# Performance work log

Hardware: AMD Instinct MI355X
Metric: run time of the kernel (lower is better)

Reference implementation:

```python
import jax, jax.numpy as jnp
import numpy as np

N_NODES = 50000
N_EDGES = 800000
IN_DIM = 162
HID = 256  # layer_1_feats == layer_2_feats (required by the stack op)


def _lin(k, fan_in, fan_out):
    kw, kb = jax.random.split(k)
    bound = 1.0 / np.sqrt(fan_in)
    w = jax.random.uniform(kw, (fan_in, fan_out), jnp.float32, -bound, bound)
    b = jax.random.uniform(kb, (fan_out,), jnp.float32, -bound, bound)
    return w, b


def setup_inputs() -> dict:
    key = jax.random.key(0)
    ks = jax.random.split(key, 12)
    feat = jax.random.normal(ks[0], (N_NODES, IN_DIM), jnp.float32)
    edge_index = jax.random.randint(ks[1], (2, N_EDGES), 0, N_NODES, jnp.int64)
    g0_w, g0_b = _lin(ks[2], IN_DIM, HID)
    g1_w, g1_b = _lin(ks[3], HID, HID)
    g2_w, g2_b = _lin(ks[4], HID, HID)
    gl_w, gl_b = _lin(ks[5], HID, HID)
    m1a_w, m1a_b = _lin(ks[6], IN_DIM, HID)
    m1b_w, m1b_b = _lin(ks[7], HID, HID)
    m2a_w, m2a_b = _lin(ks[8], HID, HID)
    m2b_w, m2b_b = _lin(ks[9], HID, HID)
    return dict(feat=feat, edge_index=edge_index,
                g0_w=g0_w, g0_b=g0_b, g1_w=g1_w, g1_b=g1_b,
                g2_w=g2_w, g2_b=g2_b, gl_w=gl_w, gl_b=gl_b,
                m1a_w=m1a_w, m1a_b=m1a_b, m1b_w=m1b_w, m1b_b=m1b_b,
                m2a_w=m2a_w, m2a_b=m2a_b, m2b_w=m2b_w, m2b_b=m2b_b)


def _gin_conv(x, src, dst, wa, ba, wb, bb):
    # DGL GINConv('sum'), eps=0: h = MLP(x + sum_{u->v} x[u])
    agg = jax.ops.segment_sum(x[src], dst, num_segments=N_NODES)
    h = jax.nn.relu((x + agg) @ wa + ba)
    return jax.nn.relu(h @ wb + bb)


def reference(feat, edge_index, g0_w, g0_b, g1_w, g1_b, g2_w, g2_b,
              gl_w, gl_b, m1a_w, m1a_b, m1b_w, m1b_b, m2a_w, m2a_b,
              m2b_w, m2b_b):
    src, dst = edge_index[0], edge_index[1]
    # layer-0 graph embedding from raw features
    g_emb0 = jax.nn.relu(jnp.sum(feat, 0) @ g0_w + g0_b)
    # GIN layer 1
    node1 = _gin_conv(feat, src, dst, m1a_w, m1a_b, m1b_w, m1b_b)
    g_emb1 = jax.nn.relu(jnp.sum(node1, 0) @ g1_w + g1_b)
    # GIN layer 2
    node2 = _gin_conv(node1, src, dst, m2a_w, m2a_b, m2b_w, m2b_b)
    g_emb2 = jax.nn.relu(jnp.sum(node2, 0) @ g2_w + g2_b)
    # sum of per-layer graph embeddings -> last linear
    g_sum = g_emb0 + g_emb1 + g_emb2
    g_last = jax.nn.relu(g_sum @ gl_w + gl_b)
    return node2 + g_last  # broadcast [N, HID] + [HID]
```

## Files before the change

### kernel.cpp

```cpp
#include <hip/hip_runtime.h>

#define N_NODES 50000
#define N_EDGES 800000
#define IN_DIM  162
#define HID     256
#define KPAD1   192
#define NB      ((N_NODES + 255) / 256)

typedef __bf16 bf16;
typedef __bf16 bf16x8 __attribute__((ext_vector_type(8)));
typedef __bf16 bf16x4 __attribute__((ext_vector_type(4)));
typedef float  f32x4  __attribute__((ext_vector_type(4)));
typedef float  f32x8  __attribute__((ext_vector_type(8)));
typedef float  f32x16 __attribute__((ext_vector_type(16)));

__device__ __forceinline__ void wf_one(const float* W, bf16* Wf, int K, int E)
{
    int e    = E & 7;
    int lane = (E >> 3) & 63;
    int fb   = (E >> 9) & 15;
    int ks   = E >> 13;
    int n = (fb >> 1) * 32 + (lane & 31);
    int k = ks * 32 + (fb & 1) * 16 + (lane >> 5) * 8 + e;
    Wf[E] = (k < K) ? (bf16)W[(size_t)k * HID + n] : (bf16)0.0f;
}

#define WTB  ((HID * KPAD1 + 3 * HID * HID + 255) / 256)
#define FPB  ((N_NODES + 63) / 64)
#define DGB  (N_EDGES / 256)

__global__ void prep_all(const float* __restrict__ m1aw, const float* __restrict__ m1bw,
                         const float* __restrict__ m2aw, const float* __restrict__ m2bw,
                         bf16* __restrict__ Wf1, bf16* __restrict__ Wf2,
                         bf16* __restrict__ Wf3, bf16* __restrict__ Wf4,
                         const float* __restrict__ feat, bf16* __restrict__ featbf,
                         float* __restrict__ colsum8,
                         const int* __restrict__ dst, int* __restrict__ deg)
{
    __shared__ bf16  tile[64][208];
    __shared__ float pcs[4][KPAD1];

    const int b   = blockIdx.x;
    const int tid = threadIdx.x;

    if (b < WTB) {
        const int R1 = HID * KPAD1;
        const int R2 = HID * HID;
        int idx = b * 256 + tid;
        if (idx < R1)                 wf_one(m1aw, Wf1, IN_DIM, idx);
        else if (idx < R1 + R2)       wf_one(m1bw, Wf2, HID, idx - R1);
        else if (idx < R1 + 2 * R2)   wf_one(m2aw, Wf3, HID, idx - R1 - R2);
        else if (idx < R1 + 3 * R2)   wf_one(m2bw, Wf4, HID, idx - R1 - 2 * R2);
        return;
    }
    if (b < WTB + FPB) {
        const int fp = b - WTB;
        const int r0 = fp * 64;

        if (tid < 192) {
            const int ch = tid % 48;
            const int rg = tid / 48;
            const int c4 = ch * 4;
            float a0 = 0.0f, a1 = 0.0f, a2 = 0.0f, a3 = 0.0f;
#pragma unroll 4
            for (int k = 0; k < 16; ++k) {
                const int rl = rg * 16 + k;
                const int r  = r0 + rl;
                bf16x4 o;
                if (r < N_NODES) {
                    const float* fr = feat + (size_t)r * IN_DIM;
                    float f0 = (c4 + 0 < IN_DIM) ? fr[c4 + 0] : 0.0f;
                    float f1 = (c4 + 1 < IN_DIM) ? fr[c4 + 1] : 0.0f;
                    float f2 = (c4 + 2 < IN_DIM) ? fr[c4 + 2] : 0.0f;
                    float f3 = (c4 + 3 < IN_DIM) ? fr[c4 + 3] : 0.0f;
                    a0 += f0; a1 += f1; a2 += f2; a3 += f3;
                    o[0] = (bf16)f0; o[1] = (bf16)f1; o[2] = (bf16)f2; o[3] = (bf16)f3;
                } else {
#pragma unroll
                    for (int j = 0; j < 4; ++j) o[j] = (bf16)0.0f;
                }
                *(bf16x4*)(&tile[rl][c4]) = o;
            }
            pcs[rg][c4 + 0] = a0;
            pcs[rg][c4 + 1] = a1;
            pcs[rg][c4 + 2] = a2;
            pcs[rg][c4 + 3] = a3;
        }
        __syncthreads();

#pragma unroll
        for (int i = 0; i < 6; ++i) {
            int m  = i * 256 + tid;
            int g  = m / 192;
            int wg = m - g * 192;
            int eo = wg * 8;
            int rl = eo / 24;
            int cc = eo - rl * 24;
            int r  = r0 + rl;
            if (r < N_NODES) {
                bf16x8 o = *(const bf16x8*)(&tile[rl][g * 24 + cc]);
                *(bf16x8*)(featbf + ((size_t)g * N_NODES + r0) * 24 + (size_t)rl * 24 + cc) = o;
            }
        }

        if (tid < IN_DIM) {
            float s = pcs[0][tid] + pcs[1][tid] + pcs[2][tid] + pcs[3][tid];
            atomicAdd(&colsum8[(fp & 7) * KPAD1 + tid], s);
        }
        return;
    }
    {
        int e = (b - WTB - FPB) * 256 + tid;
        atomicAdd(&deg[dst[e]], 1);
    }
}

__global__ void block_degsum(const int* __restrict__ deg, int* __restrict__ bsum)
{
    __shared__ int s[256];
    int t = threadIdx.x;
    int idx = blockIdx.x * 256 + t;
    int v = (idx < N_NODES) ? deg[idx] : 0;
    s[t] = v;
    __syncthreads();
    for (int off = 128; off > 0; off >>= 1) {
        if (t < off) s[t] += s[t + off];
        __syncthreads();
    }
    if (t == 0) bsum[blockIdx.x] = s[0];
}

__global__ void scan_bsum(const int* __restrict__ bsum, int* __restrict__ gsum)
{
    __shared__ int s[256];
    int t = threadIdx.x;
    int v = (t < NB) ? bsum[t] : 0;
    s[t] = v;
    __syncthreads();
    for (int off = 1; off < 256; off <<= 1) {
        int u = (t >= off) ? s[t - off] : 0;
        __syncthreads();
        s[t] += u;
        __syncthreads();
    }
    gsum[t] = s[t] - v;
}

__global__ void block_scan_write(const int* __restrict__ deg, const int* __restrict__ gsum,
                                 int* __restrict__ rowptr, int* __restrict__ cursor)
{
    __shared__ int s[256];
    int t = threadIdx.x;
    int idx = blockIdx.x * 256 + t;
    int v = (idx < N_NODES) ? deg[idx] : 0;
    s[t] = v;
    __syncthreads();
    for (int off = 1; off < 256; off <<= 1) {
        int u = (t >= off) ? s[t - off] : 0;
        __syncthreads();
        s[t] += u;
        __syncthreads();
    }
    int excl = s[t] - v + gsum[blockIdx.x];
    if (idx < N_NODES) {
        rowptr[idx] = excl;
        cursor[idx] = excl;
    }
    if (idx == 0) rowptr[N_NODES] = N_EDGES;
}

#define CFT 2048
#define NRANGE ((N_NODES + 7) / 8)

__global__ void csr_fill_b(const int* __restrict__ src, const int* __restrict__ dst,
                           int* __restrict__ cursor, int* __restrict__ csr_src)
{
    const int g    = blockIdx.x & 7;
    const int tile = blockIdx.x >> 3;
    const int lo   = g * NRANGE;
    const int hi   = lo + NRANGE;
    const int e0   = tile * CFT;
#pragma unroll
    for (int i = 0; i < CFT / 256; ++i) {
        int e = e0 + i * 256 + threadIdx.x;
        if (e < N_EDGES) {
            int d = dst[e];
            if (d >= lo && d < hi) {
                int p = atomicAdd(&cursor[d], 1);
                csr_src[p] = src[e];
            }
        }
    }
}

template<int CHUNK, int NACT>
__launch_bounds__(256)
__global__ void gather_v5(const bf16* __restrict__ xin,
                          const int* __restrict__ rowptr,
                          const int* __restrict__ csr_src,
                          bf16* __restrict__ xout)
{
    const int g    = blockIdx.x & 7;
    const int tile = blockIdx.x >> 3;
    const int wv   = threadIdx.x >> 6;
    const int lane = threadIdx.x & 63;
    const int q    = lane >> 4;
    const int j    = lane & 15;
    const int e    = j >> 2;
    const int c4   = j & 3;
    const int n    = tile * 16 + wv * 4 + q;
    const bool valid = (n < N_NODES);
    const bool act   = (c4 < NACT);
    const int  ce    = c4 * 8;
    const bf16* base = xin + (size_t)g * N_NODES * CHUNK;

    int r0 = 0, deg = 0;
    if (valid) {
        r0  = rowptr[n];
        deg = rowptr[n + 1] - r0;
    }

    int a0 = r0 + j;        if (a0 > N_EDGES - 1) a0 = N_EDGES - 1;
    int a1 = r0 + 16 + j;   if (a1 > N_EDGES - 1) a1 = N_EDGES - 1;
    const int i0 = csr_src[a0];
    const int i1 = csr_src[a1];

    f32x8 acc;
#pragma unroll
    for (int t = 0; t < 8; ++t) acc[t] = 0.0f;
    if (valid && e == 0 && act) {
        bf16x8 t0 = *(const bf16x8*)(base + (size_t)n * CHUNK + ce);
#pragma unroll
        for (int t = 0; t < 8; ++t) acc[t] = (float)t0[t];
    }

    const int lb = lane & ~3;

    {
        const int s0 = __shfl(i0, lb + 0, 64);
        const int s1 = __shfl(i0, lb + 1, 64);
        const int s2 = __shfl(i0, lb + 2, 64);
        const int s3 = __shfl(i0, lb + 3, 64);
        const int p0 = 4 * e;
        if (act) {
            bf16x8 u0 = *(const bf16x8*)(base + (size_t)s0 * CHUNK + ce);
            bf16x8 u1 = *(const bf16x8*)(base + (size_t)s1 * CHUNK + ce);
            bf16x8 u2 = *(const bf16x8*)(base + (size_t)s2 * CHUNK + ce);
            bf16x8 u3 = *(const bf16x8*)(base + (size_t)s3 * CHUNK + ce);
            if (p0 + 0 < deg) {
#pragma unroll
                for (int t = 0; t < 8; ++t) acc[t] += (float)u0[t];
            }
            if (p0 + 1 < deg) {
#pragma unroll
                for (int t = 0; t < 8; ++t) acc[t] += (float)u1[t];
            }
            if (p0 + 2 < deg) {
#pragma unroll
                for (int t = 0; t < 8; ++t) acc[t] += (float)u2[t];
            }
            if (p0 + 3 < deg) {
#pragma unroll
                for (int t = 0; t < 8; ++t) acc[t] += (float)u3[t];
            }
        }
    }

    {
        const int s0 = __shfl(i1, lb + 0, 64);
        const int s1 = __shfl(i1, lb + 1, 64);
        const int s2 = __shfl(i1, lb + 2, 64);
        const int s3 = __shfl(i1, lb + 3, 64);
        const int p0 = 16 + 4 * e;
        if (act && p0 < deg) {
            bf16x8 u0 = *(const bf16x8*)(base + (size_t)s0 * CHUNK + ce);
            bf16x8 u1 = *(const bf16x8*)(base + (size_t)s1 * CHUNK + ce);
            bf16x8 u2 = *(const bf16x8*)(base + (size_t)s2 * CHUNK + ce);
            bf16x8 u3 = *(const bf16x8*)(base + (size_t)s3 * CHUNK + ce);
            {
#pragma unroll
                for (int t = 0; t < 8; ++t) acc[t] += (float)u0[t];
            }
            if (p0 + 1 < deg) {
#pragma unroll
                for (int t = 0; t < 8; ++t) acc[t] += (float)u1[t];
            }
            if (p0 + 2 < deg) {
#pragma unroll
                for (int t = 0; t < 8; ++t) acc[t] += (float)u2[t];
            }
            if (p0 + 3 < deg) {
#pragma unroll
                for (int t = 0; t < 8; ++t) acc[t] += (float)u3[t];
            }
        }
    }

    for (int p = 32 + e; p < deg; p += 4) {
        const int s = csr_src[r0 + p];
        if (act) {
            bf16x8 u = *(const bf16x8*)(base + (size_t)s * CHUNK + ce);
#pragma unroll
            for (int t = 0; t < 8; ++t) acc[t] += (float)u[t];
        }
    }

#pragma unroll
    for (int t = 0; t < 8; ++t) {
        acc[t] += __shfl_xor(acc[t], 4, 64);
        acc[t] += __shfl_xor(acc[t], 8, 64);
    }

    if (valid && e == 0 && act) {
        bf16x8 o;
#pragma unroll
        for (int t = 0; t < 8; ++t) o[t] = (bf16)acc[t];
        __builtin_nontemporal_store(o,
            (bf16x8*)(xout + ((size_t)g * N_NODES + n) * CHUNK + ce));
    }
}

template<int KPAD, int ACHUNK, int OCHUNK>
__launch_bounds__(512)
__global__ void gemm_mlp32(const bf16* __restrict__ X,
                           const bf16* __restrict__ Wf1,
                           const float* __restrict__ bias1,
                           const bf16* __restrict__ Wf2,
                           const float* __restrict__ bias2,
                           bf16* __restrict__ out_bf,
                           float* __restrict__ colsum8,
                           int M)
{
    __shared__ __align__(128) bf16 sH[32 * HID];

    const int tid  = threadIdx.x;
    const int w    = tid >> 6;
    const int lane = tid & 63;
    const int p    = lane >> 5;
    const int cn   = lane & 31;
    const int m_base = blockIdx.x * 32;

    int arow = m_base + cn;
    if (arow >= M) arow = M - 1;

    f32x16 acc;
#pragma unroll
    for (int r = 0; r < 16; ++r) acc[r] = 0.0f;

    constexpr int T1 = KPAD / 16;
#pragma unroll
    for (int t = 0; t < T1; ++t) {
        bf16x8 a;
        {
            const int e = t * 16 + p * 8;
            if constexpr (ACHUNK == 0) {
                a = *(const bf16x8*)(X + (size_t)arow * KPAD + e);
            } else {
                const int gch = e / ACHUNK;
                const int off = e - gch * ACHUNK;
                a = *(const bf16x8*)(X + ((size_t)gch * N_NODES + arow) * ACHUNK + off);
            }
        }
        bf16x8 b = *(const bf16x8*)(Wf1 + ((((t >> 1) * 16 + w * 2 + (t & 1)) * 64) + lane) * 8);
        acc = __builtin_amdgcn_mfma_f32_32x32x16_bf16(a, b, acc, 0, 0, 0);
    }

    char* sHb = (char*)sH;
    {
        const int col = w * 32 + cn;
        const float bv = bias1[col];
#pragma unroll
        for (int r = 0; r < 16; ++r) {
            const int rowl = (r & 3) + 8 * (r >> 2) + 4 * p;
            float v = acc[r] + bv;
            v = v > 0.0f ? v : 0.0f;
            int ba = rowl * (HID * 2) + col * 2;
            ba ^= (rowl & 31) << 4;
            *(bf16*)(sHb + ba) = (bf16)v;
        }
    }
    __syncthreads();

#pragma unroll
    for (int r = 0; r < 16; ++r) acc[r] = 0.0f;

    const int hrow = cn;
    const int hswz = (hrow & 31) << 4;
    constexpr int T2 = HID / 16;
#pragma unroll
    for (int t = 0; t < T2; ++t) {
        const int kb = (t * 16 + p * 8) * 2;
        bf16x8 a = *(const bf16x8*)(sHb + ((hrow * (HID * 2) + kb) ^ hswz));
        bf16x8 b = *(const bf16x8*)(Wf2 + ((((t >> 1) * 16 + w * 2 + (t & 1)) * 64) + lane) * 8);
        acc = __builtin_amdgcn_mfma_f32_32x32x16_bf16(a, b, acc, 0, 0, 0);
    }

    {
        const int col = w * 32 + cn;
        const float bv = bias2[col];
        float part = 0.0f;
#pragma unroll
        for (int r = 0; r < 16; ++r) {
            int rl = (r & 3) + 8 * (r >> 2) + 4 * p;
            int mo = m_base + rl;
            if (mo < M) {
                float v = acc[r] + bv;
                v = v > 0.0f ? v : 0.0f;
                if constexpr (OCHUNK == 0)
                    out_bf[(size_t)mo * HID + col] = (bf16)v;
                else
                    out_bf[((size_t)w * N_NODES + mo) * OCHUNK + cn] = (bf16)v;
                part += v;
            }
        }
        if (colsum8) {
            part += __shfl_xor(part, 32, 64);
            if (p == 0) atomicAdd(&colsum8[(blockIdx.x & 7) * HID + col], part);
        }
    }
}

__global__ void graph_head(const float* __restrict__ cs0_8,
                           const float* __restrict__ cs1_8,
                           const float* __restrict__ cs2_8,
                           const float* __restrict__ g0w, const float* __restrict__ g0b,
                           const float* __restrict__ g1w, const float* __restrict__ g1b,
                           const float* __restrict__ g2w, const float* __restrict__ g2b,
                           const float* __restrict__ glw, const float* __restrict__ glb,
                           float* __restrict__ gvec)
{
    __shared__ float v0[IN_DIM], v1[HID], v2[HID], gs[HID];
    int t = threadIdx.x;
    if (t < IN_DIM) {
        float s = 0.0f;
#pragma unroll
        for (int i = 0; i < 8; ++i) s += cs0_8[i * KPAD1 + t];
        v0[t] = s;
    }
    {
        float s1 = 0.0f, s2 = 0.0f;
#pragma unroll
        for (int i = 0; i < 8; ++i) {
            s1 += cs1_8[i * HID + t];
            s2 += cs2_8[i * HID + t];
        }
        v1[t] = s1;
        v2[t] = s2;
    }
    __syncthreads();

    float a0 = 0.0f, a1 = 0.0f, a2 = 0.0f;
    for (int k = 0; k < IN_DIM; ++k) a0 += v0[k] * g0w[k * HID + t];
    for (int k = 0; k < HID; ++k) {
        a1 += v1[k] * g1w[k * HID + t];
        a2 += v2[k] * g2w[k * HID + t];
    }
    float e0 = fmaxf(a0 + g0b[t], 0.0f);
    float e1 = fmaxf(a1 + g1b[t], 0.0f);
    float e2 = fmaxf(a2 + g2b[t], 0.0f);
    gs[t] = e0 + e1 + e2;
    __syncthreads();

    float a3 = 0.0f;
    for (int k = 0; k < HID; ++k) a3 += gs[k] * glw[k * HID + t];
    gvec[t] = fmaxf(a3 + glb[t], 0.0f);
}

__global__ void final_add(const bf16* __restrict__ node2,
                          const float* __restrict__ gvec,
                          float* __restrict__ out)
{
    int idx = blockIdx.x * blockDim.x + threadIdx.x;
    size_t base = (size_t)idx * 4;
    int c = (int)(base & (HID - 1));
    bf16x4 v = *(const bf16x4*)(node2 + base);
    f32x4 g = *(const f32x4*)(gvec + c);
    f32x4 o;
#pragma unroll
    for (int j = 0; j < 4; ++j) o[j] = (float)v[j] + g[j];
    *(f32x4*)(out + base) = o;
}

extern "C" void kernel_launch(void* const* d_in, const int* in_sizes, int n_in,
                              void* d_out, int out_size, void* d_ws, size_t ws_size,
                              hipStream_t stream)
{
    const float* feat = (const float*)d_in[0];
    const int*   ei   = (const int*)d_in[1];
    const int*   src  = ei;
    const int*   dst  = ei + N_EDGES;
    const float* g0w = (const float*)d_in[2],  *g0b = (const float*)d_in[3];
    const float* g1w = (const float*)d_in[4],  *g1b = (const float*)d_in[5];
    const float* g2w = (const float*)d_in[6],  *g2b = (const float*)d_in[7];
    const float* glw = (const float*)d_in[8],  *glb = (const float*)d_in[9];
    const float* m1aw = (const float*)d_in[10], *m1ab = (const float*)d_in[11];
    const float* m1bw = (const float*)d_in[12], *m1bb = (const float*)d_in[13];
    const float* m2aw = (const float*)d_in[14], *m2ab = (const float*)d_in[15];
    const float* m2bw = (const float*)d_in[16], *m2bb = (const float*)d_in[17];
    float* out = (float*)d_out;

    char* ws = (char*)d_ws;
    size_t off = 0;
    auto alloc = [&](size_t bytes) -> void* {
        void* p = ws + off;
        off += (bytes + 255) & ~(size_t)255;
        return p;
    };
    bf16*  featbf = (bf16*)alloc((size_t)N_NODES * KPAD1 * 2);
    bf16*  xsum  = (bf16*) alloc((size_t)N_NODES * KPAD1 * 2);
    bf16*  y2    = (bf16*) alloc((size_t)N_NODES * HID * 2);
    bf16*  node2 = (bf16*) alloc((size_t)N_NODES * HID * 2);
    bf16*  node1 = (bf16*) alloc((size_t)N_NODES * HID * 2);
    bf16*  Wf1   = (bf16*) alloc((size_t)HID * KPAD1 * 2);
    bf16*  Wf2   = (bf16*) alloc((size_t)HID * HID * 2);
    bf16*  Wf3   = (bf16*) alloc((size_t)HID * HID * 2);
    bf16*  Wf4   = (bf16*) alloc((size_t)HID * HID * 2);
    int*   deg     = (int*)alloc((size_t)N_NODES * 4);
    int*   rowptr  = (int*)alloc((size_t)(N_NODES + 1) * 4);
    int*   cursor  = (int*)alloc((size_t)N_NODES * 4);
    int*   csr_src = (int*)alloc((size_t)N_EDGES * 4);
    int*   bsum    = (int*)alloc(256 * 4);
    int*   gsum    = (int*)alloc(256 * 4);
    float* csums   = (float*)alloc((8 * KPAD1 + 8 * HID + 8 * HID + HID) * 4);
    float* colsum0_8 = csums;
    float* colsum1_8 = csums + 8 * KPAD1;
    float* colsum2_8 = csums + 8 * KPAD1 + 8 * HID;
    float* gvec      = csums + 8 * KPAD1 + 16 * HID;

    hipMemsetAsync(csums, 0, (8 * KPAD1 + 16 * HID) * 4, stream);
    hipMemsetAsync(deg, 0, (size_t)N_NODES * 4, stream);

    prep_all<<<WTB + FPB + DGB, 256, 0, stream>>>(
        m1aw, m1bw, m2aw, m2bw, Wf1, Wf2, Wf3, Wf4,
        feat, featbf, colsum0_8, dst, deg);

    block_degsum<<<NB, 256, 0, stream>>>(deg, bsum);
    scan_bsum<<<1, 256, 0, stream>>>(bsum, gsum);
    block_scan_write<<<NB, 256, 0, stream>>>(deg, gsum, rowptr, cursor);
    csr_fill_b<<<((N_EDGES + CFT - 1) / CFT) * 8, 256, 0, stream>>>(src, dst, cursor, csr_src);

    const int gtiles = (N_NODES + 15) / 16;
    gather_v5<24, 3><<<gtiles * 8, 256, 0, stream>>>(featbf, rowptr, csr_src, xsum);

    const int gblocks = (N_NODES + 31) / 32;
    gemm_mlp32<KPAD1, 24, 32><<<gblocks, 512, 0, stream>>>(
        xsum, Wf1, m1ab, Wf2, m1bb, node1, colsum1_8, N_NODES);
    gather_v5<32, 4><<<gtiles * 8, 256, 0, stream>>>(node1, rowptr, csr_src, y2);
    gemm_mlp32<HID, 32, 0><<<gblocks, 512, 0, stream>>>(
        y2, Wf3, m2ab, Wf4, m2bb, node2, colsum2_8, N_NODES);
    graph_head<<<1, 256, 0, stream>>>(colsum0_8, colsum1_8, colsum2_8,
                                      g0w, g0b, g1w, g1b, g2w, g2b, glw, glb, gvec);
    final_add<<<((size_t)N_NODES * HID / 4 + 255) / 256, 256, 0, stream>>>(node2, gvec, out);
    (void)in_sizes; (void)n_in; (void)out_size; (void)ws_size;
}
```

Before: 419.3 us.

## Merge scan kernels, fuse graph head into final add, combine memsets

Replaces the three-kernel degree scan with one 1024-thread kernel where each thread scans 52 entries in registers. Fuses the graph-head MLP into the final broadcast-add: each of 256 blocks recomputes the head redundantly, then grid-strides over the output. Merges the two memsets into one by placing csums right after deg, and skips the second csr_src load when degree is at most 16. The aim is fewer kernel launches and less idle gap between them; the cost is a serial single-block scan and duplicated head work in every block.

```diff
diff --git a/kernel.cpp b/kernel.cpp
--- a/kernel.cpp
+++ b/kernel.cpp
@@ -5,7 +5,6 @@
 #define IN_DIM  162
 #define HID     256
 #define KPAD1   192
-#define NB      ((N_NODES + 255) / 256)
 
 typedef __bf16 bf16;
 typedef __bf16 bf16x8 __attribute__((ext_vector_type(8)));
@@ -115,58 +114,46 @@
     }
 }
 
-__global__ void block_degsum(const int* __restrict__ deg, int* __restrict__ bsum)
-{
-    __shared__ int s[256];
-    int t = threadIdx.x;
-    int idx = blockIdx.x * 256 + t;
-    int v = (idx < N_NODES) ? deg[idx] : 0;
-    s[t] = v;
+#define SCT 52
+__launch_bounds__(1024)
+__global__ void csr_scan(const int* __restrict__ deg,
+                         int* __restrict__ rowptr, int* __restrict__ cursor)
+{
+    __shared__ int s[1024];
+    const int t = threadIdx.x;
+    const int base = t * SCT;
+    int4 v[13];
+    int sum = 0;
+#pragma unroll
+    for (int i = 0; i < 13; ++i) {
+        int idx = base + i * 4;
+        int4 q = *(const int4*)(deg + idx);
+        q.x = (idx + 0 < N_NODES) ? q.x : 0;
+        q.y = (idx + 1 < N_NODES) ? q.y : 0;
+        q.z = (idx + 2 < N_NODES) ? q.z : 0;
+        q.w = (idx + 3 < N_NODES) ? q.w : 0;
+        v[i] = q;
+        sum += q.x + q.y + q.z + q.w;
+    }
+    s[t] = sum;
     __syncthreads();
-    for (int off = 128; off > 0; off >>= 1) {
-        if (t < off) s[t] += s[t + off];
-        __syncthreads();
-    }
-    if (t == 0) bsum[blockIdx.x] = s[0];
-}
-
-__global__ void scan_bsum(const int* __restrict__ bsum, int* __restrict__ gsum)
-{
-    __shared__ int s[256];
-    int t = threadIdx.x;
-    int v = (t < NB) ? bsum[t] : 0;
-    s[t] = v;
-    __syncthreads();
-    for (int off = 1; off < 256; off <<= 1) {
+    for (int off = 1; off < 1024; off <<= 1) {
         int u = (t >= off) ? s[t - off] : 0;
         __syncthreads();
         s[t] += u;
         __syncthreads();
     }
-    gsum[t] = s[t] - v;
-}
-
-__global__ void block_scan_write(const int* __restrict__ deg, const int* __restrict__ gsum,
-                                 int* __restrict__ rowptr, int* __restrict__ cursor)
-{
-    __shared__ int s[256];
-    int t = threadIdx.x;
-    int idx = blockIdx.x * 256 + t;
-    int v = (idx < N_NODES) ? deg[idx] : 0;
-    s[t] = v;
-    __syncthreads();
-    for (int off = 1; off < 256; off <<= 1) {
-        int u = (t >= off) ? s[t - off] : 0;
-        __syncthreads();
-        s[t] += u;
-        __syncthreads();
-    }
-    int excl = s[t] - v + gsum[blockIdx.x];
-    if (idx < N_NODES) {
-        rowptr[idx] = excl;
-        cursor[idx] = excl;
-    }
-    if (idx == 0) rowptr[N_NODES] = N_EDGES;
+    int run = s[t] - sum;
+#pragma unroll
+    for (int i = 0; i < 13; ++i) {
+        int idx = base + i * 4;
+        int4 q = v[i];
+        if (idx + 0 < N_NODES) { rowptr[idx + 0] = run; cursor[idx + 0] = run; run += q.x; }
+        if (idx + 1 < N_NODES) { rowptr[idx + 1] = run; cursor[idx + 1] = run; run += q.y; }
+        if (idx + 2 < N_NODES) { rowptr[idx + 2] = run; cursor[idx + 2] = run; run += q.z; }
+        if (idx + 3 < N_NODES) { rowptr[idx + 3] = run; cursor[idx + 3] = run; run += q.w; }
+    }
+    if (t == 1023) rowptr[N_NODES] = N_EDGES;
 }
 
 #define CFT 2048
@@ -223,7 +210,8 @@
     int a0 = r0 + j;        if (a0 > N_EDGES - 1) a0 = N_EDGES - 1;
     int a1 = r0 + 16 + j;   if (a1 > N_EDGES - 1) a1 = N_EDGES - 1;
     const int i0 = csr_src[a0];
-    const int i1 = csr_src[a1];
+    int i1 = 0;
+    if (deg > 16) i1 = csr_src[a1];
 
     f32x8 acc;
 #pragma unroll
@@ -420,17 +408,19 @@
     }
 }
 
-__global__ void graph_head(const float* __restrict__ cs0_8,
-                           const float* __restrict__ cs1_8,
-                           const float* __restrict__ cs2_8,
-                           const float* __restrict__ g0w, const float* __restrict__ g0b,
-                           const float* __restrict__ g1w, const float* __restrict__ g1b,
-                           const float* __restrict__ g2w, const float* __restrict__ g2b,
-                           const float* __restrict__ glw, const float* __restrict__ glb,
-                           float* __restrict__ gvec)
-{
-    __shared__ float v0[IN_DIM], v1[HID], v2[HID], gs[HID];
-    int t = threadIdx.x;
+__launch_bounds__(256)
+__global__ void final_gh(const float* __restrict__ cs0_8,
+                         const float* __restrict__ cs1_8,
+                         const float* __restrict__ cs2_8,
+                         const float* __restrict__ g0w, const float* __restrict__ g0b,
+                         const float* __restrict__ g1w, const float* __restrict__ g1b,
+                         const float* __restrict__ g2w, const float* __restrict__ g2b,
+                         const float* __restrict__ glw, const float* __restrict__ glb,
+                         const bf16* __restrict__ node2,
+                         float* __restrict__ out)
+{
+    __shared__ float v0[IN_DIM], v1[HID], v2[HID], gs[HID], gv[HID];
+    const int t = threadIdx.x;
     if (t < IN_DIM) {
         float s = 0.0f;
 #pragma unroll
@@ -463,22 +453,19 @@
 
     float a3 = 0.0f;
     for (int k = 0; k < HID; ++k) a3 += gs[k] * glw[k * HID + t];
-    gvec[t] = fmaxf(a3 + glb[t], 0.0f);
-}
-
-__global__ void final_add(const bf16* __restrict__ node2,
-                          const float* __restrict__ gvec,
-                          float* __restrict__ out)
-{
-    int idx = blockIdx.x * blockDim.x + threadIdx.x;
-    size_t base = (size_t)idx * 4;
-    int c = (int)(base & (HID - 1));
-    bf16x4 v = *(const bf16x4*)(node2 + base);
-    f32x4 g = *(const f32x4*)(gvec + c);
-    f32x4 o;
-#pragma unroll
-    for (int j = 0; j < 4; ++j) o[j] = (float)v[j] + g[j];
-    *(f32x4*)(out + base) = o;
+    gv[t] = fmaxf(a3 + glb[t], 0.0f);
+    __syncthreads();
+
+    const int total = N_NODES * HID / 4;
+    for (int q = blockIdx.x * 256 + t; q < total; q += gridDim.x * 256) {
+        size_t bb = (size_t)q * 4;
+        int c = (int)(bb & (HID - 1));
+        bf16x4 v = *(const bf16x4*)(node2 + bb);
+        f32x4 o;
+#pragma unroll
+        for (int jj = 0; jj < 4; ++jj) o[jj] = (float)v[jj] + gv[c + jj];
+        *(f32x4*)(out + bb) = o;
+    }
 }
 
 extern "C" void kernel_launch(void* const* d_in, const int* in_sizes, int n_in,
@@ -515,28 +502,23 @@
     bf16*  Wf2   = (bf16*) alloc((size_t)HID * HID * 2);
     bf16*  Wf3   = (bf16*) alloc((size_t)HID * HID * 2);
     bf16*  Wf4   = (bf16*) alloc((size_t)HID * HID * 2);
-    int*   deg     = (int*)alloc((size_t)N_NODES * 4);
+    int*   deg   = (int*)  alloc((size_t)N_NODES * 4);
+    float* csums = (float*)alloc((8 * KPAD1 + 16 * HID) * 4);
     int*   rowptr  = (int*)alloc((size_t)(N_NODES + 1) * 4);
     int*   cursor  = (int*)alloc((size_t)N_NODES * 4);
     int*   csr_src = (int*)alloc((size_t)N_EDGES * 4);
-    int*   bsum    = (int*)alloc(256 * 4);
-    int*   gsum    = (int*)alloc(256 * 4);
-    float* csums   = (float*)alloc((8 * KPAD1 + 8 * HID + 8 * HID + HID) * 4);
     float* colsum0_8 = csums;
     float* colsum1_8 = csums + 8 * KPAD1;
     float* colsum2_8 = csums + 8 * KPAD1 + 8 * HID;
-    float* gvec      = csums + 8 * KPAD1 + 16 * HID;
-
-    hipMemsetAsync(csums, 0, (8 * KPAD1 + 16 * HID) * 4, stream);
-    hipMemsetAsync(deg, 0, (size_t)N_NODES * 4, stream);
+
+    const size_t deg_pad = (((size_t)N_NODES * 4) + 255) & ~(size_t)255;
+    hipMemsetAsync(deg, 0, deg_pad + (8 * KPAD1 + 16 * HID) * 4, stream);
 
     prep_all<<<WTB + FPB + DGB, 256, 0, stream>>>(
         m1aw, m1bw, m2aw, m2bw, Wf1, Wf2, Wf3, Wf4,
         feat, featbf, colsum0_8, dst, deg);
 
-    block_degsum<<<NB, 256, 0, stream>>>(deg, bsum);
-    scan_bsum<<<1, 256, 0, stream>>>(bsum, gsum);
-    block_scan_write<<<NB, 256, 0, stream>>>(deg, gsum, rowptr, cursor);
+    csr_scan<<<1, 1024, 0, stream>>>(deg, rowptr, cursor);
     csr_fill_b<<<((N_EDGES + CFT - 1) / CFT) * 8, 256, 0, stream>>>(src, dst, cursor, csr_src);
 
     const int gtiles = (N_NODES + 15) / 16;
@@ -548,8 +530,8 @@
     gather_v5<32, 4><<<gtiles * 8, 256, 0, stream>>>(node1, rowptr, csr_src, y2);
     gemm_mlp32<HID, 32, 0><<<gblocks, 512, 0, stream>>>(
         y2, Wf3, m2ab, Wf4, m2bb, node2, colsum2_8, N_NODES);
-    graph_head<<<1, 256, 0, stream>>>(colsum0_8, colsum1_8, colsum2_8,
-                                      g0w, g0b, g1w, g1b, g2w, g2b, glw, glb, gvec);
-    final_add<<<((size_t)N_NODES * HID / 4 + 255) / 256, 256, 0, stream>>>(node2, gvec, out);
+    final_gh<<<256, 256, 0, stream>>>(colsum0_8, colsum1_8, colsum2_8,
+                                      g0w, g0b, g1w, g1b, g2w, g2b, glw, glb,
+                                      node2, out);
     (void)in_sizes; (void)n_in; (void)out_size; (void)ws_size;
 }
```

After: 464.8 us. 1.11x slower.
